# Kernel optimization log

Measured on AMD Instinct MI355X. Metric: run time of the kernel, lower is better.

The kernel has to match this reference:

```python
import jax, jax.numpy as jnp
import numpy as np

TEMPERATURE = 0.1
EPS = 1e-12  # matches torch F.normalize default eps


def setup_inputs() -> dict:
    key = jax.random.key(0)
    k1, k2 = jax.random.split(key)
    B, D = 4096, 512
    features1 = jax.random.normal(k1, (B, D), dtype=jnp.float32)
    features2 = jax.random.normal(k2, (B, D), dtype=jnp.float32)
    return {"features1": features1, "features2": features2}


def _l2_normalize(x, axis=1):
    norm = jnp.linalg.norm(x, axis=axis, keepdims=True)
    return x / jnp.maximum(norm, EPS)


def reference(features1, features2):
    B = features1.shape[0]
    f1 = _l2_normalize(features1)
    f2 = _l2_normalize(features2)
    features = jnp.concatenate([f1, f2], axis=0)  # (2B, D)
    sim = jnp.matmul(features, features.T) / TEMPERATURE  # (2B, 2B)
    # mask self-similarity on the diagonal with -inf
    diag = jnp.eye(2 * B, dtype=bool)
    sim = jnp.where(diag, -jnp.inf, sim)
    # positive pair labels: row i pairs with i+B (first half) / i-B (second half)
    labels = jnp.concatenate([jnp.arange(B) + B, jnp.arange(B)], axis=0)
    log_probs = jax.nn.log_softmax(sim, axis=-1)  # (2B, 2B)
    nll = -jnp.take_along_axis(log_probs, labels[:, None], axis=1)[:, 0]
    return jnp.mean(nll)
```

## Files before the change

### kernel.cpp

```cpp
#include <hip/hip_runtime.h>

#define NROWS 8192
#define HALF_N 4096
#define DIM 512
#define INV_T 10.0f
#define NRB 64
#define NBLOCKS 2080

typedef __attribute__((ext_vector_type(4))) float f32x4;
typedef __attribute__((ext_vector_type(2))) long long2v;

__device__ __forceinline__ void async16(const void* g, void* l) {
  __builtin_amdgcn_global_load_lds(
      (const __attribute__((address_space(1))) unsigned int*)g,
      (__attribute__((address_space(3))) unsigned int*)l, 16, 0, 0);
}

__global__ __launch_bounds__(256) void norm_cast_k(
    const float* __restrict__ f1, const float* __restrict__ f2,
    unsigned char* __restrict__ Fa, unsigned char* __restrict__ Fb,
    float* __restrict__ rowsum, float* __restrict__ out) {
  int wave = threadIdx.x >> 6;
  int lane = threadIdx.x & 63;
  int row = blockIdx.x * 4 + wave;
  const float* src = (row < HALF_N) ? (f1 + (size_t)row * DIM)
                                    : (f2 + (size_t)(row - HALF_N) * DIM);
  const float4* p = reinterpret_cast<const float4*>(src + lane * 8);
  float4 v0 = p[0];
  float4 v1 = p[1];
  float ss = v0.x*v0.x + v0.y*v0.y + v0.z*v0.z + v0.w*v0.w
           + v1.x*v1.x + v1.y*v1.y + v1.z*v1.z + v1.w*v1.w;
  #pragma unroll
  for (int off = 1; off < 64; off <<= 1) ss += __shfl_xor(ss, off);
  float scale = 1.0f / fmaxf(sqrtf(ss), 1e-12f);
  int lo = __builtin_amdgcn_cvt_pk_fp8_f32(v0.x * scale, v0.y * scale, 0, false);
  lo = __builtin_amdgcn_cvt_pk_fp8_f32(v0.z * scale, v0.w * scale, lo, true);
  int hi = __builtin_amdgcn_cvt_pk_fp8_f32(v1.x * scale, v1.y * scale, 0, false);
  hi = __builtin_amdgcn_cvt_pk_fp8_f32(v1.z * scale, v1.w * scale, hi, true);
  int2 val = make_int2(lo, hi);
  int u = lane & 7;
  int g = lane >> 3;
  int pos = 2 * (u & 3) + (u >> 2);
  *reinterpret_cast<int2*>(Fb + (size_t)row * DIM + g * 64 + pos * 8) = val;
  int chunk = g * 4 + (u & 3);
  int slot = u >> 2;
  *reinterpret_cast<int2*>(Fa + (size_t)(row >> 4) * 8192 + chunk * 256 +
                           (row & 15) * 16 + slot * 8) = val;
  if (lane == 0) rowsum[row] = 0.0f;
  if (blockIdx.x == 0 && threadIdx.x == 0) out[0] = 0.0f;
}

__global__ __launch_bounds__(256, 3) void sym_gemm_k(
    const unsigned char* __restrict__ Fa, const unsigned char* __restrict__ Fb,
    float* __restrict__ rowsum, float* __restrict__ pairsim) {
  int bx = blockIdx.x;
  int gbx = (bx & 7) * (NBLOCKS / 8) + (bx >> 3);
  int rb = 0, rem = gbx;
  while (rem >= NRB - rb) { rem -= NRB - rb; ++rb; }
  const int cb = rb + rem;
  const int row0 = rb * 128, col0 = cb * 128;

  const int tid = threadIdx.x;
  const int wave = tid >> 6;
  const int lane = tid & 63;
  const int quad = lane >> 4;
  const int colid = lane & 15;
  const int wr0 = (wave >> 1) * 64;
  const int wc0 = (wave & 1) * 64;

  __shared__ __align__(16) unsigned char Blds[128 * 64];
  __shared__ float redrow[128];
  __shared__ float redcol[128];

  if (tid < 128) { redrow[tid] = 0.0f; redcol[tid] = 0.0f; }

  const unsigned char* srcB[2]; unsigned char* dstB[2];
  #pragma unroll
  for (int seg = 0; seg < 2; ++seg) {
    int inst = wave + seg * 4;
    int r = inst * 16 + (lane >> 2);
    int c = (lane & 3) ^ ((r >> 1) & 3);
    srcB[seg] = Fb + (size_t)(col0 + r) * DIM + c * 16;
    dstB[seg] = Blds + inst * 1024;
  }

  const unsigned char* agp[4];
  #pragma unroll
  for (int t = 0; t < 4; ++t)
    agp[t] = Fa + (size_t)((row0 + wr0 + t * 16) >> 4) * 8192 +
             quad * 256 + colid * 16;

  const unsigned char* bfp[4];
  #pragma unroll
  for (int t = 0; t < 4; ++t) {
    int rc = wc0 + t * 16 + colid;
    bfp[t] = Blds + rc * 64 + ((quad ^ ((rc >> 1) & 3)) << 4);
  }

  f32x4 acc[4][4];
  #pragma unroll
  for (int t = 0; t < 4; ++t)
    #pragma unroll
    for (int u = 0; u < 4; ++u) acc[t][u] = (f32x4){0.f, 0.f, 0.f, 0.f};

  for (int kc = 0; kc < 8; ++kc) {
    __syncthreads();
    const size_t ko = (size_t)kc * 64;
    #pragma unroll
    for (int seg = 0; seg < 2; ++seg)
      async16(srcB[seg] + ko, dstB[seg]);
    long2v af[4];
    #pragma unroll
    for (int t = 0; t < 4; ++t)
      af[t] = *reinterpret_cast<const long2v*>(agp[t] + kc * 1024);
    __syncthreads();

    long2v bf[4];
    #pragma unroll
    for (int u = 0; u < 4; ++u) bf[u] = *reinterpret_cast<const long2v*>(bfp[u]);
    #pragma unroll
    for (int s = 0; s < 2; ++s)
      #pragma unroll
      for (int t = 0; t < 4; ++t)
        #pragma unroll
        for (int u = 0; u < 4; ++u)
          acc[t][u] = __builtin_amdgcn_mfma_f32_16x16x32_fp8_fp8(
              af[t][s], bf[u][s], acc[t][u], 0, 0, 0);
  }

  float re[4][4];
  float ce[4];
  #pragma unroll
  for (int t = 0; t < 4; ++t)
    #pragma unroll
    for (int r = 0; r < 4; ++r) re[t][r] = 0.0f;
  #pragma unroll
  for (int u = 0; u < 4; ++u) ce[u] = 0.0f;

  #pragma unroll
  for (int t = 0; t < 4; ++t) {
    #pragma unroll
    for (int u = 0; u < 4; ++u) {
      f32x4 a = acc[t][u];
      const int gc = col0 + wc0 + u * 16 + colid;
      #pragma unroll
      for (int r = 0; r < 4; ++r) {
        int grow = row0 + wr0 + t * 16 + quad * 4 + r;
        float sim = a[r] * INV_T;
        float e = (gc > grow) ? __expf(sim) : 0.0f;
        re[t][r] += e;
        ce[u] += e;
        if (gc == grow + HALF_N && grow < HALF_N) {
          pairsim[grow] = sim;
          pairsim[gc] = sim;
        }
      }
    }
  }

  #pragma unroll
  for (int t = 0; t < 4; ++t)
    #pragma unroll
    for (int r = 0; r < 4; ++r) {
      float v = re[t][r];
      v += __shfl_xor(v, 1); v += __shfl_xor(v, 2);
      v += __shfl_xor(v, 4); v += __shfl_xor(v, 8);
      if (colid == 0) atomicAdd(&redrow[wr0 + t * 16 + quad * 4 + r], v);
    }
  #pragma unroll
  for (int u = 0; u < 4; ++u) {
    float v = ce[u];
    v += __shfl_xor(v, 16); v += __shfl_xor(v, 32);
    if (lane < 16) atomicAdd(&redcol[wc0 + u * 16 + colid], v);
  }
  __syncthreads();
  if (tid < 128) atomicAdd(&rowsum[row0 + tid], redrow[tid]);
  else           atomicAdd(&rowsum[col0 + tid - 128], redcol[tid - 128]);
}

__global__ __launch_bounds__(256) void finalize_k(
    const float* __restrict__ rowsum, const float* __restrict__ pairsim,
    float* __restrict__ out) {
  int i = blockIdx.x * 256 + threadIdx.x;
  float local = logf(rowsum[i]) - pairsim[i];
  #pragma unroll
  for (int off = 1; off < 64; off <<= 1) local += __shfl_xor(local, off);
  if ((threadIdx.x & 63) == 0)
    atomicAdd(out, local * (1.0f / (float)NROWS));
}

extern "C" void kernel_launch(void* const* d_in, const int* in_sizes, int n_in,
                              void* d_out, int out_size, void* d_ws, size_t ws_size,
                              hipStream_t stream) {
  const float* f1 = (const float*)d_in[0];
  const float* f2 = (const float*)d_in[1];
  unsigned char* Fa = (unsigned char*)d_ws;
  unsigned char* Fb = Fa + (size_t)NROWS * DIM;
  float* rowsum = (float*)(Fb + (size_t)NROWS * DIM);
  float* pairsim = rowsum + NROWS;
  float* out = (float*)d_out;

  norm_cast_k<<<NROWS / 4, 256, 0, stream>>>(f1, f2, Fa, Fb, rowsum, out);
  sym_gemm_k<<<NBLOCKS, 256, 0, stream>>>(Fa, Fb, rowsum, pairsim);
  finalize_k<<<NROWS / 256, 256, 0, stream>>>(rowsum, pairsim, out);
}
```

Before: 104.8 us.

## Load both GEMM operands directly from global fragments, drop LDS staging

The B operand is no longer staged through shared memory. It is read straight from the same pre-swizzled fragment layout used for A, so the second layout copy and its write in the normalize kernel go away. The k-loop now prefetches the next chunk's A and B fragments into registers while the MFMAs run, and the two barriers per iteration are removed. The cost is more global/L2 traffic per block, since each wave fetches its own B fragments instead of sharing them through LDS, plus extra registers for the prefetch buffers.

```diff
diff --git a/kernel.cpp b/kernel.cpp
--- a/kernel.cpp
+++ b/kernel.cpp
@@ -10,16 +10,10 @@
 typedef __attribute__((ext_vector_type(4))) float f32x4;
 typedef __attribute__((ext_vector_type(2))) long long2v;
 
-__device__ __forceinline__ void async16(const void* g, void* l) {
-  __builtin_amdgcn_global_load_lds(
-      (const __attribute__((address_space(1))) unsigned int*)g,
-      (__attribute__((address_space(3))) unsigned int*)l, 16, 0, 0);
-}
-
 __global__ __launch_bounds__(256) void norm_cast_k(
     const float* __restrict__ f1, const float* __restrict__ f2,
-    unsigned char* __restrict__ Fa, unsigned char* __restrict__ Fb,
-    float* __restrict__ rowsum, float* __restrict__ out) {
+    unsigned char* __restrict__ Fa, float* __restrict__ rowsum,
+    float* __restrict__ out) {
   int wave = threadIdx.x >> 6;
   int lane = threadIdx.x & 63;
   int row = blockIdx.x * 4 + wave;
@@ -40,8 +34,6 @@
   int2 val = make_int2(lo, hi);
   int u = lane & 7;
   int g = lane >> 3;
-  int pos = 2 * (u & 3) + (u >> 2);
-  *reinterpret_cast<int2*>(Fb + (size_t)row * DIM + g * 64 + pos * 8) = val;
   int chunk = g * 4 + (u & 3);
   int slot = u >> 2;
   *reinterpret_cast<int2*>(Fa + (size_t)(row >> 4) * 8192 + chunk * 256 +
@@ -51,7 +43,7 @@
 }
 
 __global__ __launch_bounds__(256, 3) void sym_gemm_k(
-    const unsigned char* __restrict__ Fa, const unsigned char* __restrict__ Fb,
+    const unsigned char* __restrict__ Fa,
     float* __restrict__ rowsum, float* __restrict__ pairsim) {
   int bx = blockIdx.x;
   int gbx = (bx & 7) * (NBLOCKS / 8) + (bx >> 3);
@@ -68,33 +60,19 @@
   const int wr0 = (wave >> 1) * 64;
   const int wc0 = (wave & 1) * 64;
 
-  __shared__ __align__(16) unsigned char Blds[128 * 64];
   __shared__ float redrow[128];
   __shared__ float redcol[128];
-
-  if (tid < 128) { redrow[tid] = 0.0f; redcol[tid] = 0.0f; }
-
-  const unsigned char* srcB[2]; unsigned char* dstB[2];
-  #pragma unroll
-  for (int seg = 0; seg < 2; ++seg) {
-    int inst = wave + seg * 4;
-    int r = inst * 16 + (lane >> 2);
-    int c = (lane & 3) ^ ((r >> 1) & 3);
-    srcB[seg] = Fb + (size_t)(col0 + r) * DIM + c * 16;
-    dstB[seg] = Blds + inst * 1024;
-  }
+  if (tid < 128) redrow[tid] = 0.0f;
+  else           redcol[tid - 128] = 0.0f;
 
   const unsigned char* agp[4];
+  const unsigned char* bgp[4];
   #pragma unroll
-  for (int t = 0; t < 4; ++t)
+  for (int t = 0; t < 4; ++t) {
     agp[t] = Fa + (size_t)((row0 + wr0 + t * 16) >> 4) * 8192 +
              quad * 256 + colid * 16;
-
-  const unsigned char* bfp[4];
-  #pragma unroll
-  for (int t = 0; t < 4; ++t) {
-    int rc = wc0 + t * 16 + colid;
-    bfp[t] = Blds + rc * 64 + ((quad ^ ((rc >> 1) & 3)) << 4);
+    bgp[t] = Fa + (size_t)((col0 + wc0 + t * 16) >> 4) * 8192 +
+             quad * 256 + colid * 16;
   }
 
   f32x4 acc[4][4];
@@ -103,21 +81,25 @@
     #pragma unroll
     for (int u = 0; u < 4; ++u) acc[t][u] = (f32x4){0.f, 0.f, 0.f, 0.f};
 
+  long2v af[4], bf[4];
+  #pragma unroll
+  for (int t = 0; t < 4; ++t)
+    af[t] = *reinterpret_cast<const long2v*>(agp[t]);
+  #pragma unroll
+  for (int u = 0; u < 4; ++u)
+    bf[u] = *reinterpret_cast<const long2v*>(bgp[u]);
+
+  #pragma unroll
   for (int kc = 0; kc < 8; ++kc) {
-    __syncthreads();
-    const size_t ko = (size_t)kc * 64;
-    #pragma unroll
-    for (int seg = 0; seg < 2; ++seg)
-      async16(srcB[seg] + ko, dstB[seg]);
-    long2v af[4];
-    #pragma unroll
-    for (int t = 0; t < 4; ++t)
-      af[t] = *reinterpret_cast<const long2v*>(agp[t] + kc * 1024);
-    __syncthreads();
-
-    long2v bf[4];
-    #pragma unroll
-    for (int u = 0; u < 4; ++u) bf[u] = *reinterpret_cast<const long2v*>(bfp[u]);
+    long2v afn[4], bfn[4];
+    if (kc < 7) {
+      #pragma unroll
+      for (int t = 0; t < 4; ++t)
+        afn[t] = *reinterpret_cast<const long2v*>(agp[t] + (kc + 1) * 1024);
+      #pragma unroll
+      for (int u = 0; u < 4; ++u)
+        bfn[u] = *reinterpret_cast<const long2v*>(bgp[u] + (kc + 1) * 1024);
+    }
     #pragma unroll
     for (int s = 0; s < 2; ++s)
       #pragma unroll
@@ -126,7 +108,15 @@
         for (int u = 0; u < 4; ++u)
           acc[t][u] = __builtin_amdgcn_mfma_f32_16x16x32_fp8_fp8(
               af[t][s], bf[u][s], acc[t][u], 0, 0, 0);
+    if (kc < 7) {
+      #pragma unroll
+      for (int t = 0; t < 4; ++t) af[t] = afn[t];
+      #pragma unroll
+      for (int u = 0; u < 4; ++u) bf[u] = bfn[u];
+    }
   }
+
+  __syncthreads();
 
   float re[4][4];
   float ce[4];
@@ -195,12 +185,11 @@
   const float* f1 = (const float*)d_in[0];
   const float* f2 = (const float*)d_in[1];
   unsigned char* Fa = (unsigned char*)d_ws;
-  unsigned char* Fb = Fa + (size_t)NROWS * DIM;
-  float* rowsum = (float*)(Fb + (size_t)NROWS * DIM);
+  float* rowsum = (float*)(Fa + (size_t)NROWS * DIM);
   float* pairsim = rowsum + NROWS;
   float* out = (float*)d_out;
 
-  norm_cast_k<<<NROWS / 4, 256, 0, stream>>>(f1, f2, Fa, Fb, rowsum, out);
-  sym_gemm_k<<<NBLOCKS, 256, 0, stream>>>(Fa, Fb, rowsum, pairsim);
+  norm_cast_k<<<NROWS / 4, 256, 0, stream>>>(f1, f2, Fa, rowsum, out);
+  sym_gemm_k<<<NBLOCKS, 256, 0, stream>>>(Fa, rowsum, pairsim);
   finalize_k<<<NROWS / 256, 256, 0, stream>>>(rowsum, pairsim, out);
 }
```

Result: slower. 107.2 us (+2.2%).
